# Kernel tuning notes

Hardware: AMD Instinct MI355X
Metric: run time of the kernel (lower is better)

Reference implementation:

```python
import jax, jax.numpy as jnp
import numpy as np

T, HID, H = 1024, 2048, 16
LQ, LKV = 1536, 512
DR, DN, DQ, DV = 64, 128, 192, 128
HI, DI, TOPK = 16, 128, 256
EPS = 1e-6
NEG = -1e30


def _rms(x, g, eps=EPS):
    return x * jax.lax.rsqrt(jnp.mean(x * x, -1, keepdims=True) + eps) * g


def _ln(x, w, b, eps=1e-6):
    m = jnp.mean(x, -1, keepdims=True)
    v = jnp.mean((x - m) ** 2, -1, keepdims=True)
    return (x - m) * jax.lax.rsqrt(v + eps) * w + b


def _rope_interleave(x, cos, sin):
    # HF apply_rotary_pos_emb_interleave: de-interleave even/odd then standard rotate_half.
    x1, x2 = x[..., 0::2], x[..., 1::2]
    xr = jnp.concatenate([x1, x2], -1)
    rot = jnp.concatenate([-x2, x1], -1)
    return xr * cos + rot * sin


def _sparse_indices(hidden, q_lat, cos, sin, ks, ke, i_wqb, i_wk, i_ln_w, i_ln_b, i_wproj):
    # hidden [T,HID], q_lat [T,LQ]; returns [T,TOPK] int32 (sentinel index = T)
    t = hidden.shape[0]
    q_idx = (q_lat @ i_wqb.T).reshape(t, HI, DI)
    k_idx = _ln(hidden @ i_wk.T, i_ln_w, i_ln_b)          # [T,DI]
    w = hidden @ i_wproj.T                                 # [T,HI]
    q_pe = _rope_interleave(q_idx[..., :DR], cos[:, None, :], sin[:, None, :])
    k_pe = _rope_interleave(k_idx[..., :DR], cos, sin)
    qi = jnp.concatenate([q_pe, q_idx[..., DR:]], -1)      # [T,HI,DI]
    ki = jnp.concatenate([k_pe, k_idx[..., DR:]], -1)      # [T,DI]
    weight_scale = DI ** -0.5 * HI ** -0.5
    logits = jnp.einsum('thd,sd->ths', qi, ki)             # [T,HI,T]
    score = jnp.einsum('ths,th->ts', jax.nn.relu(logits), w) * weight_scale
    pos = jnp.arange(t)
    valid = (pos[None, :] >= ks[:, None]) & (pos[None, :] <= ke[:, None])
    score = jnp.where(valid, score, NEG)
    vals, idx = jax.lax.top_k(score, TOPK)
    return jnp.where(vals <= NEG / 2, t, idx).astype(jnp.int32)


def reference(hidden_states, cos, sin, ks, ke,
              w_qa, g_qa, w_qb, w_kva, g_kva, w_kvb, w_o,
              i_wqb, i_wk, i_ln_w, i_ln_b, i_wproj):
    t = hidden_states.shape[1]
    # low-rank projections
    q_lat = _rms(hidden_states @ w_qa.T, g_qa)             # [1,T,LQ]
    ckv = hidden_states @ w_kva.T                          # [1,T,LKV+DR]
    k_c = _rms(ckv[..., :LKV], g_kva)                      # [1,T,LKV]
    k_r = _rope_interleave(ckv[..., LKV:], cos[None], sin[None])  # [1,T,DR]
    # fp8 indexer (reference math in fp32), no-grad in original
    indices = _sparse_indices(hidden_states[0], q_lat[0], cos, sin, ks, ke,
                              i_wqb, i_wk, i_ln_w, i_ln_b, i_wproj)  # [T,TOPK]
    # MLA up-proj with weight absorption
    q_full = (q_lat @ w_qb.T).reshape(1, t, H, DQ)
    q_nope, q_rope = q_full[..., :DN], q_full[..., DN:]
    q_rope = _rope_interleave(q_rope, cos[None, :, None, :], sin[None, :, None, :])
    w_b = w_kvb.reshape(H, DN + DV, LKV)
    w_kn, w_v = w_b[:, :DN, :], w_b[:, DN:, :]
    q_abs = jnp.einsum('bshd,hdk->bshk', q_nope, w_kn)     # absorb k_nope up-proj
    sq = jnp.concatenate([q_abs, q_rope], -1)[0]           # [T,H,LKV+DR]
    skv = jnp.concatenate([k_c, k_r], -1)[0]               # [T,LKV+DR]
    skv = jnp.concatenate([skv, jnp.zeros((1, LKV + DR), skv.dtype)], 0)  # sentinel row
    # sparse attention over gathered top-k KV rows
    kv_g = skv[indices]                                    # [T,TOPK,LKV+DR]
    logits = jnp.einsum('thd,tjd->thj', sq, kv_g) * (DQ ** -0.5)
    logits = jnp.where(indices[:, None, :] == t, NEG, logits)
    p = jax.nn.softmax(logits, -1)
    out = jnp.einsum('thj,tjk->thk', p, kv_g[..., :LKV])   # values = compressed kv
    o = jnp.einsum('thk,hdk->thd', out, w_v)               # un-absorb v up-proj
    return o.reshape(1, t, H * DV) @ w_o.T


def setup_inputs() -> dict:
    key = jax.random.key(0)
    k = jax.random.split(key, 12)
    n = lambda kk, shape, s: jax.random.normal(kk, shape, jnp.float32) * s
    pos = jnp.arange(T, dtype=jnp.float32)
    inv = 1.0 / (10000.0 ** (jnp.arange(0, DR, 2, dtype=jnp.float32) / DR))
    ang = pos[:, None] * inv[None, :]
    cos = jnp.concatenate([jnp.cos(ang), jnp.cos(ang)], -1)
    sin = jnp.concatenate([jnp.sin(ang), jnp.sin(ang)], -1)
    return dict(
        hidden_states=n(k[0], (1, T, HID), 1.0),
        cos=cos, sin=sin,
        ks=jnp.zeros((T,), jnp.int32),
        ke=jnp.arange(T, dtype=jnp.int32),  # causal: keys s <= t valid
        w_qa=n(k[1], (LQ, HID), HID ** -0.5),
        g_qa=jnp.ones((LQ,), jnp.float32),
        w_qb=n(k[2], (H * DQ, LQ), LQ ** -0.5),
        w_kva=n(k[3], (LKV + DR, HID), HID ** -0.5),
        g_kva=jnp.ones((LKV,), jnp.float32),
        w_kvb=n(k[4], (H * (DN + DV), LKV), LKV ** -0.5),
        w_o=n(k[5], (HID, H * DV), (H * DV) ** -0.5),
        i_wqb=n(k[6], (HI * DI, LQ), LQ ** -0.5),
        i_wk=n(k[7], (DI, HID), HID ** -0.5),
        i_ln_w=jnp.ones((DI,), jnp.float32),
        i_ln_b=jnp.zeros((DI,), jnp.float32),
        i_wproj=n(k[8], (HI, HID), HID ** -0.5),
    )
```

## Files before the change

kernel.cpp:

```cpp
#include <hip/hip_runtime.h>
#include <hip/hip_bf16.h>
#include <cmath>

#define T_ 1024
#define HID_ 2048
#define H_ 16
#define LQ_ 1536
#define LKV_ 512
#define DR_ 64
#define DN_ 128
#define DQ_ 192
#define DV_ 128
#define HI_ 16
#define DI_ 128
#define TOPK_ 256
#define NEGF (-1e30f)

typedef short bfrag_t __attribute__((ext_vector_type(8)));
typedef float f32x4 __attribute__((ext_vector_type(4)));

__device__ __forceinline__ float wave_sum64(float v) {
#pragma unroll
  for (int off = 32; off; off >>= 1) v += __shfl_xor(v, off);
  return v;
}

#define GLL(g, l) __builtin_amdgcn_global_load_lds((const __attribute__((address_space(1))) void*)(g), \
                                     (__attribute__((address_space(3))) void*)(l), 16, 0, 0)

__global__ __launch_bounds__(256) void zero_k(float4* __restrict__ p, int n4) {
  int i = blockIdx.x * 256 + threadIdx.x;
  if (i < n4) p[i] = make_float4(0.f, 0.f, 0.f, 0.f);
}

template<typename CT>
__global__ __launch_bounds__(256) void gemm_bf_k(
    const short* __restrict__ A, int lda, long long sA,
    const short* __restrict__ B, int ldb, long long sB,
    CT* __restrict__ C, int ldc, long long sC,
    int Nout, int K)
{
  __shared__ short As[2][128 * 32];
  __shared__ short Bs[2][128 * 32];
  A += (long long)blockIdx.z * sA;
  B += (long long)blockIdx.z * sB;
  C += (long long)blockIdx.z * sC;
  const int tid = threadIdx.x;
  const int bm = blockIdx.y * 128, bn = blockIdx.x * 128;
  const int wave = tid >> 6, lane = tid & 63;
  const int wm = (wave >> 1) * 64, wn = (wave & 1) * 64;
  const int sr = tid >> 2;
  const int scol = (tid & 3) * 8;
  const int m0 = lane & 15, koff = (lane >> 4) * 8;
  f32x4 acc[4][4] = {};
  const short* ga = A + (long long)(bm + sr) * lda + scol;
  const short* gb = B + (long long)(bn + sr) * ldb + scol;
#define STAGE_BF(buf, off) \
    GLL(ga + (off), As[buf] + tid * 8); GLL(ga + (off) + 64 * lda, As[buf] + tid * 8 + 2048); \
    GLL(gb + (off), Bs[buf] + tid * 8); GLL(gb + (off) + 64 * ldb, Bs[buf] + tid * 8 + 2048);
  const int niter = K >> 5;
  STAGE_BF(0, 0);
  for (int it = 0; it < niter; ++it) {
    const int cur = it & 1;
    if (it + 1 < niter) {
      STAGE_BF(cur ^ 1, (it + 1) * 32);
      asm volatile("s_waitcnt vmcnt(4)\ns_barrier" ::: "memory");
    } else {
      asm volatile("s_waitcnt vmcnt(0)\ns_barrier" ::: "memory");
    }
    bfrag_t af[4], bfv[4];
#pragma unroll
    for (int i = 0; i < 4; ++i)
      af[i] = *(const bfrag_t*)(As[cur] + (wm + i * 16 + m0) * 32 + koff);
#pragma unroll
    for (int j = 0; j < 4; ++j)
      bfv[j] = *(const bfrag_t*)(Bs[cur] + (wn + j * 16 + m0) * 32 + koff);
#pragma unroll
    for (int i = 0; i < 4; ++i)
#pragma unroll
      for (int j = 0; j < 4; ++j)
        acc[i][j] = __builtin_amdgcn_mfma_f32_16x16x32_bf16(af[i], bfv[j], acc[i][j], 0, 0, 0);
    asm volatile("s_barrier" ::: "memory");
  }
#undef STAGE_BF
  const int cr = (lane >> 4) * 4, cc = lane & 15;
#pragma unroll
  for (int i = 0; i < 4; ++i) {
    int row = bm + wm + i * 16 + cr;
#pragma unroll
    for (int j = 0; j < 4; ++j) {
      int col = bn + wn + j * 16 + cc;
      if (col < Nout) {
#pragma unroll
        for (int r = 0; r < 4; ++r)
          C[(long long)(row + r) * ldc + col] = (CT)(acc[i][j][r]);
      }
    }
  }
}

__global__ __launch_bounds__(256) void gemm_bfs_k(
    const short* __restrict__ A, int lda,
    const short* __restrict__ B, int ldb,
    float* __restrict__ C, int ldc, int Nout, int K)
{
  __shared__ short As[2][128 * 32];
  __shared__ short Bs[2][128 * 32];
  const long long kbase = (long long)blockIdx.z * K;
  const int tid = threadIdx.x;
  const int bm = blockIdx.y * 128, bn = blockIdx.x * 128;
  const int wave = tid >> 6, lane = tid & 63;
  const int wm = (wave >> 1) * 64, wn = (wave & 1) * 64;
  const int sr = tid >> 2;
  const int scol = (tid & 3) * 8;
  const int m0 = lane & 15, koff = (lane >> 4) * 8;
  f32x4 acc[4][4] = {};
  const short* ga = A + (long long)(bm + sr) * lda + kbase + scol;
  const short* gb = B + (long long)(bn + sr) * ldb + kbase + scol;
#define STAGE_BS(buf, off) \
    GLL(ga + (off), As[buf] + tid * 8); GLL(ga + (off) + 64 * lda, As[buf] + tid * 8 + 2048); \
    GLL(gb + (off), Bs[buf] + tid * 8); GLL(gb + (off) + 64 * ldb, Bs[buf] + tid * 8 + 2048);
  const int niter = K >> 5;
  STAGE_BS(0, 0);
  for (int it = 0; it < niter; ++it) {
    const int cur = it & 1;
    if (it + 1 < niter) {
      STAGE_BS(cur ^ 1, (it + 1) * 32);
      asm volatile("s_waitcnt vmcnt(4)\ns_barrier" ::: "memory");
    } else {
      asm volatile("s_waitcnt vmcnt(0)\ns_barrier" ::: "memory");
    }
    bfrag_t af[4], bfv[4];
#pragma unroll
    for (int i = 0; i < 4; ++i)
      af[i] = *(const bfrag_t*)(As[cur] + (wm + i * 16 + m0) * 32 + koff);
#pragma unroll
    for (int j = 0; j < 4; ++j)
      bfv[j] = *(const bfrag_t*)(Bs[cur] + (wn + j * 16 + m0) * 32 + koff);
#pragma unroll
    for (int i = 0; i < 4; ++i)
#pragma unroll
      for (int j = 0; j < 4; ++j)
        acc[i][j] = __builtin_amdgcn_mfma_f32_16x16x32_bf16(af[i], bfv[j], acc[i][j], 0, 0, 0);
    asm volatile("s_barrier" ::: "memory");
  }
#undef STAGE_BS
  const int cr = (lane >> 4) * 4, cc = lane & 15;
#pragma unroll
  for (int i = 0; i < 4; ++i) {
    int row = bm + wm + i * 16 + cr;
#pragma unroll
    for (int j = 0; j < 4; ++j) {
      int col = bn + wn + j * 16 + cc;
      if (col < Nout) {
#pragma unroll
        for (int r = 0; r < 4; ++r)
          atomicAdd(&C[(long long)(row + r) * ldc + col], acc[i][j][r]);
      }
    }
  }
}

__global__ __launch_bounds__(256) void gemm3_k(
    const short* __restrict__ Ah, const short* __restrict__ Al, int lda,
    const short* __restrict__ Bh, const short* __restrict__ Bl, int ldb,
    float* __restrict__ C, int ldc, int Nout, int K)
{
  __shared__ short Ahs[2][128 * 32];
  __shared__ short Als[2][128 * 32];
  __shared__ short Bhs[2][128 * 32];
  __shared__ short Bls[2][128 * 32];
  const long long kbase = (long long)blockIdx.z * K;
  const int tid = threadIdx.x;
  const int bm = blockIdx.y * 128, bn = blockIdx.x * 128;
  const int wave = tid >> 6, lane = tid & 63;
  const int wm = (wave >> 1) * 64, wn = (wave & 1) * 64;
  const int sr = tid >> 2;
  const int scol = (tid & 3) * 8;
  const int m0 = lane & 15, koff = (lane >> 4) * 8;
  f32x4 acc[4][4] = {};
  const short* gah = Ah + (long long)(bm + sr) * lda + kbase + scol;
  const short* gal = Al + (long long)(bm + sr) * lda + kbase + scol;
  const short* gbh = Bh + (long long)(bn + sr) * ldb + kbase + scol;
  const short* gbl = Bl + (long long)(bn + sr) * ldb + kbase + scol;
#define STAGE_3(buf, off) \
    GLL(gah + (off), Ahs[buf] + tid * 8); GLL(gah + (off) + 64 * lda, Ahs[buf] + tid * 8 + 2048); \
    GLL(gal + (off), Als[buf] + tid * 8); GLL(gal + (off) + 64 * lda, Als[buf] + tid * 8 + 2048); \
    GLL(gbh + (off), Bhs[buf] + tid * 8); GLL(gbh + (off) + 64 * ldb, Bhs[buf] + tid * 8 + 2048); \
    GLL(gbl + (off), Bls[buf] + tid * 8); GLL(gbl + (off) + 64 * ldb, Bls[buf] + tid * 8 + 2048);
  const int niter = K >> 5;
  STAGE_3(0, 0);
  for (int it = 0; it < niter; ++it) {
    const int cur = it & 1;
    if (it + 1 < niter) {
      STAGE_3(cur ^ 1, (it + 1) * 32);
      asm volatile("s_waitcnt vmcnt(8)\ns_barrier" ::: "memory");
    } else {
      asm volatile("s_waitcnt vmcnt(0)\ns_barrier" ::: "memory");
    }
    bfrag_t afh[4], afl[4], bfh[4], bfl[4];
#pragma unroll
    for (int i = 0; i < 4; ++i) {
      afh[i] = *(const bfrag_t*)(Ahs[cur] + (wm + i * 16 + m0) * 32 + koff);
      afl[i] = *(const bfrag_t*)(Als[cur] + (wm + i * 16 + m0) * 32 + koff);
    }
#pragma unroll
    for (int j = 0; j < 4; ++j) {
      bfh[j] = *(const bfrag_t*)(Bhs[cur] + (wn + j * 16 + m0) * 32 + koff);
      bfl[j] = *(const bfrag_t*)(Bls[cur] + (wn + j * 16 + m0) * 32 + koff);
    }
#pragma unroll
    for (int i = 0; i < 4; ++i)
#pragma unroll
      for (int j = 0; j < 4; ++j)
        acc[i][j] = __builtin_amdgcn_mfma_f32_16x16x32_bf16(afh[i], bfh[j], acc[i][j], 0, 0, 0);
#pragma unroll
    for (int i = 0; i < 4; ++i)
#pragma unroll
      for (int j = 0; j < 4; ++j)
        acc[i][j] = __builtin_amdgcn_mfma_f32_16x16x32_bf16(afh[i], bfl[j], acc[i][j], 0, 0, 0);
#pragma unroll
    for (int i = 0; i < 4; ++i)
#pragma unroll
      for (int j = 0; j < 4; ++j)
        acc[i][j] = __builtin_amdgcn_mfma_f32_16x16x32_bf16(afl[i], bfh[j], acc[i][j], 0, 0, 0);
    asm volatile("s_barrier" ::: "memory");
  }
#undef STAGE_3
  const int cr = (lane >> 4) * 4, cc = lane & 15;
  const bool spl = (gridDim.z > 1);
#pragma unroll
  for (int i = 0; i < 4; ++i) {
    int row = bm + wm + i * 16 + cr;
#pragma unroll
    for (int j = 0; j < 4; ++j) {
      int col = bn + wn + j * 16 + cc;
      if (col < Nout) {
#pragma unroll
        for (int r = 0; r < 4; ++r) {
          if (spl) atomicAdd(&C[(long long)(row + r) * ldc + col], acc[i][j][r]);
          else     C[(long long)(row + r) * ldc + col] = acc[i][j][r];
        }
      }
    }
  }
}

__global__ __launch_bounds__(256) void cast_bf16_k(const float* __restrict__ src,
                                                   __hip_bfloat16* __restrict__ dst, int n4) {
  int i = blockIdx.x * 256 + threadIdx.x;
  if (i >= n4) return;
  float4 v = ((const float4*)src)[i];
  union { ushort4 u; __hip_bfloat16 h[4]; } o;
  o.h[0] = __float2bfloat16(v.x); o.h[1] = __float2bfloat16(v.y);
  o.h[2] = __float2bfloat16(v.z); o.h[3] = __float2bfloat16(v.w);
  ((ushort4*)dst)[i] = o.u;
}

__global__ __launch_bounds__(256) void decomp_k(const float* __restrict__ src,
                                                __hip_bfloat16* __restrict__ hi,
                                                __hip_bfloat16* __restrict__ lo, int n4) {
  int i = blockIdx.x * 256 + threadIdx.x;
  if (i >= n4) return;
  float4 v = ((const float4*)src)[i];
  float f[4] = {v.x, v.y, v.z, v.w};
  union { ushort4 u; __hip_bfloat16 h[4]; } oh, ol;
#pragma unroll
  for (int j = 0; j < 4; ++j) {
    __hip_bfloat16 h = __float2bfloat16(f[j]);
    oh.h[j] = h;
    ol.h[j] = __float2bfloat16(f[j] - __bfloat162float(h));
  }
  ((ushort4*)hi)[i] = oh.u;
  ((ushort4*)lo)[i] = ol.u;
}

__global__ __launch_bounds__(256) void cast_pad_k(const float* __restrict__ src,
                                                  __hip_bfloat16* __restrict__ dst,
                                                  int N, int K4, int Npad) {
  int i = blockIdx.x * 256 + threadIdx.x;
  if (i >= Npad * K4) return;
  int r = i / K4;
  float4 v = make_float4(0.f, 0.f, 0.f, 0.f);
  if (r < N) v = ((const float4*)src)[i];
  union { ushort4 u; __hip_bfloat16 h[4]; } o;
  o.h[0] = __float2bfloat16(v.x); o.h[1] = __float2bfloat16(v.y);
  o.h[2] = __float2bfloat16(v.z); o.h[3] = __float2bfloat16(v.w);
  ((ushort4*)dst)[i] = o.u;
}

__global__ __launch_bounds__(256) void wkn_t_k(const float* __restrict__ wkvb,
                                               __hip_bfloat16* __restrict__ dst) {
  __shared__ float tile[64][65];
  const int h = blockIdx.z, k0 = blockIdx.y * 64, d0 = blockIdx.x * 64;
  const int c = threadIdx.x & 63, r0 = threadIdx.x >> 6;
#pragma unroll
  for (int rr = 0; rr < 16; ++rr) {
    int r = r0 + rr * 4;
    tile[r][c] = wkvb[((h * 256 + d0 + r) << 9) + k0 + c];
  }
  __syncthreads();
#pragma unroll
  for (int rr = 0; rr < 16; ++rr) {
    int r = r0 + rr * 4;
    dst[((h * 512 + k0 + r) << 7) + d0 + c] = __float2bfloat16(tile[c][r]);
  }
}

__global__ __launch_bounds__(256) void wv_cast_k(const float* __restrict__ wkvb,
                                                 __hip_bfloat16* __restrict__ dst) {
  int i = blockIdx.x * 256 + threadIdx.x;
  int k = i & 511, dv = (i >> 9) & 127, h = i >> 16;
  dst[i] = __float2bfloat16(wkvb[((h * 256 + 128 + dv) << 9) + k]);
}

__global__ __launch_bounds__(256) void rms_inplace_k(float* x, const float* __restrict__ g,
                                                     int C) {
  int t = blockIdx.x, tid = threadIdx.x;
  float* row = x + (long long)t * C;
  float ss = 0.f;
  for (int i = tid; i < C; i += 256) { float v = row[i]; ss += v * v; }
  __shared__ float red[4];
  ss = wave_sum64(ss);
  if ((tid & 63) == 0) red[tid >> 6] = ss;
  __syncthreads();
  float sc = rsqrtf((red[0] + red[1] + red[2] + red[3]) / (float)C + 1e-6f);
  for (int i = tid; i < C; i += 256) row[i] = row[i] * sc * g[i];
}

__global__ __launch_bounds__(256) void skv_build_k(const float* __restrict__ ckv,
                                                   const float* __restrict__ g,
                                                   const float* __restrict__ cosb,
                                                   const float* __restrict__ sinb,
                                                   __hip_bfloat16* __restrict__ skv) {
  int t = blockIdx.x, tid = threadIdx.x;
  __hip_bfloat16* out = skv + (long long)t * 576;
  if (t == T_) { for (int i = tid; i < 576; i += 256) out[i] = __float2bfloat16(0.f); return; }
  const float* row = ckv + (long long)t * 576;
  float ss = 0.f;
  for (int i = tid; i < 512; i += 256) { float v = row[i]; ss += v * v; }
  __shared__ float red[4];
  ss = wave_sum64(ss);
  if ((tid & 63) == 0) red[tid >> 6] = ss;
  __syncthreads();
  float sc = rsqrtf((red[0] + red[1] + red[2] + red[3]) / 512.f + 1e-6f);
  for (int i = tid; i < 512; i += 256) out[i] = __float2bfloat16(row[i] * sc * g[i]);
  if (tid < 64) {
    int j = tid, j2 = tid & 31;
    float c = cosb[t * 64 + j], s = sinb[t * 64 + j];
    float a = row[512 + 2 * j2], b = row[512 + 2 * j2 + 1];
    out[512 + j] = __float2bfloat16((j < 32) ? (a * c - b * s) : (a * s + b * c));
  }
}

__global__ __launch_bounds__(64) void rope_qi_k(float* qi, const float* __restrict__ cosb,
                                                const float* __restrict__ sinb) {
  int b = blockIdx.x, t = b >> 4, j = threadIdx.x, j2 = j & 31;
  float* x = qi + (long long)b * DI_;
  float c = cosb[t * 64 + j], s = sinb[t * 64 + j];
  float a = x[2 * j2], bb = x[2 * j2 + 1];
  float o = (j < 32) ? (a * c - bb * s) : (a * s + bb * c);
  x[j] = o;
}

__global__ __launch_bounds__(128) void ki_ln_rope_k(float* kbuf, const float* __restrict__ w,
                                                    const float* __restrict__ bia,
                                                    const float* __restrict__ cosb,
                                                    const float* __restrict__ sinb) {
  int t = blockIdx.x, i = threadIdx.x;
  float* row = kbuf + (long long)t * DI_;
  float x = row[i];
  __shared__ float red[2];
  float s1 = wave_sum64(x);
  if ((i & 63) == 0) red[i >> 6] = s1;
  __syncthreads();
  float mean = (red[0] + red[1]) / 128.f;
  float d = x - mean;
  __syncthreads();
  float s2 = wave_sum64(d * d);
  if ((i & 63) == 0) red[i >> 6] = s2;
  __syncthreads();
  float var = (red[0] + red[1]) / 128.f;
  float y = d * rsqrtf(var + 1e-6f) * w[i] + bia[i];
  __shared__ float rowl[128];
  rowl[i] = y;
  __syncthreads();
  float outv = y;
  if (i < 64) {
    int j2 = i & 31;
    float c = cosb[t * 64 + i], s = sinb[t * 64 + i];
    float a = rowl[2 * j2], b = rowl[2 * j2 + 1];
    outv = (i < 32) ? (a * c - b * s) : (a * s + b * c);
  }
  row[i] = outv;
}

__global__ __launch_bounds__(64) void rope_q_sq_k(const __hip_bfloat16* __restrict__ qfull,
                                                  const float* __restrict__ cosb,
                                                  const float* __restrict__ sinb,
                                                  __hip_bfloat16* __restrict__ sq) {
  int b = blockIdx.x, t = b >> 4, h = b & 15, j = threadIdx.x, j2 = j & 31;
  const __hip_bfloat16* x = qfull + (long long)t * 3072 + h * 192 + 128;
  float c = cosb[t * 64 + j], s = sinb[t * 64 + j];
  float a = __bfloat162float(x[2 * j2]), bb = __bfloat162float(x[2 * j2 + 1]);
  float o = (j < 32) ? (a * c - bb * s) : (a * s + bb * c);
  sq[((long long)t * H_ + h) * 576 + 512 + j] = __float2bfloat16(o);
}

__global__ __launch_bounds__(256) void wproj_k(const float* __restrict__ hidden,
                                               const float* __restrict__ wp,
                                               float* __restrict__ out) {
  int wave = threadIdx.x >> 6, lane = threadIdx.x & 63;
  int t = blockIdx.x * 4 + wave;
  const float4* x4 = (const float4*)(hidden + (long long)t * 2048);
  float acc[16] = {};
  for (int c = lane; c < 512; c += 64) {
    float4 xv = x4[c];
#pragma unroll
    for (int h = 0; h < 16; ++h) {
      float4 wv = ((const float4*)(wp + h * 2048))[c];
      acc[h] += xv.x * wv.x + xv.y * wv.y + xv.z * wv.z + xv.w * wv.w;
    }
  }
#pragma unroll
  for (int h = 0; h < 16; ++h) {
    float s = wave_sum64(acc[h]);
    if (lane == 0) out[t * 16 + h] = s;
  }
}

__global__ __launch_bounds__(256) void score_k(
    const short* __restrict__ qi_hi, const short* __restrict__ qi_lo,
    const short* __restrict__ ki_hi, const short* __restrict__ ki_lo,
    const float* __restrict__ wproj, const int* __restrict__ ks,
    const int* __restrict__ ke, float* __restrict__ scores)
{
  __shared__ float s_w[HI_];
  const int seg = blockIdx.x, t = blockIdx.y, tid = threadIdx.x;
  const int wave = tid >> 6, lane = tid & 63;
  const int m0 = lane & 15, quad = lane >> 4;
  if (tid < HI_) s_w[tid] = wproj[t * HI_ + tid] * 0.022097086912079608f;
  __syncthreads();

  bfrag_t ah[4], al[4];
  {
    const short* qh = qi_hi + ((long long)t * HI_ + m0) * DI_ + quad * 8;
    const short* ql = qi_lo + ((long long)t * HI_ + m0) * DI_ + quad * 8;
#pragma unroll
    for (int k = 0; k < 4; ++k) {
      ah[k] = *(const bfrag_t*)(qh + k * 32);
      al[k] = *(const bfrag_t*)(ql + k * 32);
    }
  }
  const int lo = ks[t], hi = ke[t];
  float* srow = scores + t * T_;
#pragma unroll
  for (int tt = 0; tt < 4; ++tt) {
    const int n0 = seg * 256 + wave * 64 + tt * 16;
    const short* kh = ki_hi + (n0 + m0) * DI_ + quad * 8;
    const short* kl = ki_lo + (n0 + m0) * DI_ + quad * 8;
    bfrag_t bh[4], bl[4];
#pragma unroll
    for (int k = 0; k < 4; ++k) {
      bh[k] = *(const bfrag_t*)(kh + k * 32);
      bl[k] = *(const bfrag_t*)(kl + k * 32);
    }
    f32x4 acc = {0.f, 0.f, 0.f, 0.f};
#pragma unroll
    for (int k = 0; k < 4; ++k) {
      acc = __builtin_amdgcn_mfma_f32_16x16x32_bf16(ah[k], bh[k], acc, 0, 0, 0);
      acc = __builtin_amdgcn_mfma_f32_16x16x32_bf16(ah[k], bl[k], acc, 0, 0, 0);
      acc = __builtin_amdgcn_mfma_f32_16x16x32_bf16(al[k], bh[k], acc, 0, 0, 0);
    }
    float sc = 0.f;
#pragma unroll
    for (int r = 0; r < 4; ++r) sc += fmaxf(acc[r], 0.f) * s_w[quad * 4 + r];
    sc += __shfl_xor(sc, 16);
    sc += __shfl_xor(sc, 32);
    if (quad == 0) {
      int key = n0 + m0;
      srow[key] = (key >= lo && key <= hi) ? sc : NEGF;
    }
  }
}

__global__ __launch_bounds__(256) void topk_k(const float* __restrict__ scores,
                                              int* __restrict__ indices)
{
  __shared__ unsigned s_hist[256];
  __shared__ unsigned s_wsum[4];
  __shared__ unsigned s_binsel[2];
  __shared__ unsigned s_cnt;
  const int t = blockIdx.x, tid = threadIdx.x;
  const int wave = tid >> 6, lane = tid & 63;
  const int i0 = tid * 4;
  if (tid == 0) s_cnt = 0;

  float4 sv = ((const float4*)(scores + t * T_))[tid];
  float f[4] = {sv.x, sv.y, sv.z, sv.w};
  unsigned key[4];
#pragma unroll
  for (int j = 0; j < 4; ++j) {
    unsigned u = __float_as_uint(f[j]);
    key[j] = (u & 0x80000000u) ? ~u : (u | 0x80000000u);
  }

  unsigned prefix = 0, Gprev = 0;
  for (int lvl = 0; lvl < 4; ++lvl) {
    const int shift = 24 - 8 * lvl;
    s_hist[tid] = 0;
    __syncthreads();
#pragma unroll
    for (int j = 0; j < 4; ++j) {
      unsigned k = key[j];
      bool part = (lvl == 0) || ((k >> (shift + 8)) == prefix);
      unsigned bin = (k >> shift) & 255u;
      unsigned long long mask = __ballot(part);
#pragma unroll
      for (int b = 0; b < 8; ++b) {
        unsigned long long bal = __ballot((bin >> b) & 1u);
        mask &= ((bin >> b) & 1u) ? bal : ~bal;
      }
      if (part && lane == (__ffsll((long long)mask) - 1))
        atomicAdd(&s_hist[bin], (unsigned)__popcll(mask));
    }
    __syncthreads();
    unsigned h = s_hist[255 - tid];
    unsigned sc_ = h;
    for (int off = 1; off < 64; off <<= 1) {
      unsigned v = __shfl_up(sc_, off);
      if (lane >= off) sc_ += v;
    }
    if (lane == 63) s_wsum[wave] = sc_;
    __syncthreads();
    unsigned wo = 0;
    for (int w = 0; w < wave; ++w) wo += s_wsum[w];
    unsigned incl = sc_ + wo, excl = incl - h;
    unsigned Rn = 256 - Gprev;
    if (excl < Rn && Rn <= incl) { s_binsel[0] = 255 - (unsigned)tid; s_binsel[1] = excl; }
    __syncthreads();
    prefix = (prefix << 8) | s_binsel[0];
    Gprev += s_binsel[1];
  }
  const unsigned thr = prefix;
  const unsigned Rq = 256 - Gprev;
  const unsigned negfkey = ~__float_as_uint(NEGF);

  unsigned eqc = 0;
#pragma unroll
  for (int j = 0; j < 4; ++j) eqc += (key[j] == thr) ? 1u : 0u;
  unsigned esc = eqc;
  for (int off = 1; off < 64; off <<= 1) {
    unsigned v = __shfl_up(esc, off);
    if (lane >= off) esc += v;
  }
  if (lane == 63) s_wsum[wave] = esc;
  __syncthreads();
  unsigned eo = 0;
  for (int w = 0; w < wave; ++w) eo += s_wsum[w];
  unsigned rank = esc + eo - eqc;

#pragma unroll
  for (int j = 0; j < 4; ++j) {
    unsigned k = key[j];
    int outv = (k == negfkey) ? T_ : (i0 + j);
    bool gt = (k > thr);
    unsigned long long bal = __ballot(gt);
    if (bal) {
      int leader = __ffsll((long long)bal) - 1;
      unsigned base = 0;
      if (lane == leader) base = atomicAdd(&s_cnt, (unsigned)__popcll(bal));
      base = (unsigned)__shfl((int)base, leader);
      if (gt) {
        unsigned pre = (unsigned)__popcll(bal & ((1ull << lane) - 1ull));
        indices[t * TOPK_ + base + pre] = outv;
      }
    }
    if (!gt && k == thr) {
      if (rank < Rq) indices[t * TOPK_ + Gprev + rank] = outv;
      rank++;
    }
  }
}

#define SP_LD 257
#define PB_LD 264
#define VT_LD 264
__global__ __launch_bounds__(512) void attn_k(
    const short* __restrict__ sq, const short* __restrict__ skv,
    const int* __restrict__ indices, __hip_bfloat16* __restrict__ attn_out)
{
  __shared__ int s_ind[TOPK_];
  __shared__ __align__(16) char s_un[2 * 64 * VT_LD * 2];
  float* s_p  = (float*)s_un;
  short* s_pb = (short*)(s_un + 16448);
  short* s_vt = (short*)s_un;
  const int t = blockIdx.x, tid = threadIdx.x;
  const int wave = tid >> 6, lane = tid & 63;
  const int m0 = lane & 15, quad = lane >> 4;
  if (tid < TOPK_) s_ind[tid] = indices[t * TOPK_ + tid];
  __syncthreads();

  {
    const int jb = wave * 32;
    int rows[2];
    const short* kvp[2];
#pragma unroll
    for (int j = 0; j < 2; ++j) {
      rows[j] = s_ind[jb + j * 16 + m0];
      kvp[j] = skv + rows[j] * 576 + quad * 8;
    }
    const short* qp = sq + ((long long)t * H_ + m0) * 576 + quad * 8;
    f32x4 qacc[2] = {};
    for (int ks = 0; ks < 18; ++ks) {
      const int k0 = ks * 32;
      bfrag_t aq = *(const bfrag_t*)(qp + k0);
#pragma unroll
      for (int j = 0; j < 2; ++j) {
        bfrag_t bq = *(const bfrag_t*)(kvp[j] + k0);
        qacc[j] = __builtin_amdgcn_mfma_f32_16x16x32_bf16(aq, bq, qacc[j], 0, 0, 0);
      }
    }
    const float scale = 0.07216878364870322f;
#pragma unroll
    for (int j = 0; j < 2; ++j) {
      int key = jb + j * 16 + m0;
      bool msk = (rows[j] == T_);
#pragma unroll
      for (int r = 0; r < 4; ++r)
        s_p[(quad * 4 + r) * SP_LD + key] = msk ? NEGF : qacc[j][r] * scale;
    }
  }
  __syncthreads();

  for (int h = wave * 2; h < wave * 2 + 2; ++h) {
    float* ph = s_p + h * SP_LD;
    float m = -3.4e38f;
    for (int j = lane; j < TOPK_; j += 64) m = fmaxf(m, ph[j]);
#pragma unroll
    for (int off = 32; off; off >>= 1) m = fmaxf(m, __shfl_xor(m, off));
    float sum = 0.f;
    for (int j = lane; j < TOPK_; j += 64) {
      float e = __expf(ph[j] - m);
      ph[j] = e; sum += e;
    }
    sum = wave_sum64(sum);
    float inv = 1.f / sum;
    for (int j = lane; j < TOPK_; j += 64) ph[j] *= inv;
  }
  __syncthreads();

  {
    const int col = tid & 255, h0 = tid >> 8;
#pragma unroll
    for (int h = 0; h < 8; ++h) {
      const int hh = h0 + h * 2;
      s_pb[hh * PB_LD + col] =
          (short)__bfloat16_as_ushort(__float2bfloat16(s_p[hh * SP_LD + col]));
    }
  }
  __syncthreads();

  bfrag_t apf[8];
#pragma unroll
  for (int kk = 0; kk < 8; ++kk)
    apf[kk] = *(const bfrag_t*)(s_pb + m0 * PB_LD + kk * 32 + quad * 8);

  const int grp = wave >> 2, gw = wave & 3;
  short* svt = s_vt + grp * (64 * VT_LD);
  const int r8 = (tid >> 3) & 31;
  const int bb = tid & 7;

  for (int cc = 0; cc < 4; ++cc) {
    const int c = grp * 4 + cc;
    __syncthreads();
#pragma unroll
    for (int rep = 0; rep < 8; ++rep) {
      const int kv = r8 + 32 * rep;
      const int row = s_ind[kv];
      bfrag_t v = *(const bfrag_t*)(skv + (long long)row * 576 + c * 64 + bb * 8);
      const int colx = kv ^ (bb << 3);
#pragma unroll
      for (int j = 0; j < 8; ++j)
        svt[(bb * 8 + j) * VT_LD + colx] = v[j];
    }
    __syncthreads();
    const int d = gw * 16 + m0;
    const short* vrow = svt + d * VT_LD;
    const int sx = (d >> 3) << 3;
    f32x4 oacc = {0.f, 0.f, 0.f, 0.f};
#pragma unroll
    for (int kk = 0; kk < 8; ++kk) {
      bfrag_t bv = *(const bfrag_t*)(vrow + ((kk * 32 + quad * 8) ^ sx));
      oacc = __builtin_amdgcn_mfma_f32_16x16x32_bf16(apf[kk], bv, oacc, 0, 0, 0);
    }
    const int col = c * 64 + d;
#pragma unroll
    for (int r = 0; r < 4; ++r)
      attn_out[((long long)t * H_ + quad * 4 + r) * 512 + col] = __float2bfloat16(oacc[r]);
  }
}

extern "C" void kernel_launch(void* const* d_in, const int* in_sizes, int n_in,
                              void* d_out, int out_size, void* d_ws, size_t ws_size,
                              hipStream_t stream) {
  const float* hidden  = (const float*)d_in[0];
  const float* cosb    = (const float*)d_in[1];
  const float* sinb    = (const float*)d_in[2];
  const int*   ks      = (const int*)d_in[3];
  const int*   ke      = (const int*)d_in[4];
  const float* w_qa    = (const float*)d_in[5];
  const float* g_qa    = (const float*)d_in[6];
  const float* w_qb    = (const float*)d_in[7];
  const float* w_kva   = (const float*)d_in[8];
  const float* g_kva   = (const float*)d_in[9];
  const float* w_kvb   = (const float*)d_in[10];
  const float* w_o     = (const float*)d_in[11];
  const float* i_wqb   = (const float*)d_in[12];
  const float* i_wk    = (const float*)d_in[13];
  const float* i_ln_w  = (const float*)d_in[14];
  const float* i_ln_b  = (const float*)d_in[15];
  const float* i_wproj = (const float*)d_in[16];
  float* out = (float*)d_out;
  (void)in_sizes; (void)n_in; (void)out_size; (void)ws_size;

  char* ws = (char*)d_ws;
  __hip_bfloat16* hid_hi  = (__hip_bfloat16*)(ws + 0);
  __hip_bfloat16* hid_lo  = (__hip_bfloat16*)(ws + 4194304);
  float*          q_lat   = (float*)(ws + 8388608);
  __hip_bfloat16* qi_hi   = (__hip_bfloat16*)(ws + 8388608);
  __hip_bfloat16* qlat_hi = (__hip_bfloat16*)(ws + 14680064);
  __hip_bfloat16* qlat_lo = (__hip_bfloat16*)(ws + 17825792);
  float*          qi      = (float*)(ws + 20971520);
  float*          scoresb = (float*)(ws + 20971520);
  float*          kib     = (float*)(ws + 29360128);
  float*          wbuf    = (float*)(ws + 29884416);
  float*          ckv     = (float*)(ws + 29949952);
  __hip_bfloat16* qi_lo   = (__hip_bfloat16*)(ws + 29949952);
  __hip_bfloat16* ki_hi   = (__hip_bfloat16*)(ws + 34144256);
  __hip_bfloat16* ki_lo   = (__hip_bfloat16*)(ws + 34406400);
  __hip_bfloat16* sq_bf   = (__hip_bfloat16*)(ws + 0);
  __hip_bfloat16* o_bf    = (__hip_bfloat16*)(ws + 0);
  __hip_bfloat16* W       = (__hip_bfloat16*)(ws + 37748736);
  __hip_bfloat16* skv_bf  = (__hip_bfloat16*)(ws + 47185920);
  int*            idxb    = (int*)(ws + 48366720);
  __hip_bfloat16* E       = (__hip_bfloat16*)(ws + 49415296);

  dim3 blk(256);
  const short* Ws = (const short*)W;
  const short* Es = (const short*)E;

  decomp_k<<<2048, blk, 0, stream>>>(hidden, hid_hi, hid_lo, 524288);

  decomp_k<<<3072, blk, 0, stream>>>(w_qa, W, E, 786432);
  zero_k<<<1536, blk, 0, stream>>>((float4*)q_lat, 393216);
  gemm3_k<<<dim3(12, 8, 4), blk, 0, stream>>>(
      (const short*)hid_hi, (const short*)hid_lo, HID_, Ws, Es, HID_, q_lat, LQ_, LQ_, 512);
  rms_inplace_k<<<T_, blk, 0, stream>>>(q_lat, g_qa, LQ_);

  cast_pad_k<<<1280, blk, 0, stream>>>(w_kva, W, 576, 512, 640);
  zero_k<<<576, blk, 0, stream>>>((float4*)ckv, 147456);
  gemm_bfs_k<<<dim3(5, 8, 4), blk, 0, stream>>>(
      (const short*)hid_hi, HID_, Ws, HID_, ckv, 576, 576, 512);
  skv_build_k<<<T_ + 1, blk, 0, stream>>>(ckv, g_kva, cosb, sinb, skv_bf);

  decomp_k<<<1536, blk, 0, stream>>>(q_lat, qlat_hi, qlat_lo, 393216);

  decomp_k<<<3072, blk, 0, stream>>>(i_wqb, W, E, 786432);
  zero_k<<<2048, blk, 0, stream>>>((float4*)qi, 524288);
  gemm3_k<<<dim3(16, 8, 4), blk, 0, stream>>>(
      (const short*)qlat_hi, (const short*)qlat_lo, LQ_, Ws, Es, LQ_, qi, HI_ * DI_, HI_ * DI_, 384);
  rope_qi_k<<<T_ * HI_, dim3(64), 0, stream>>>(qi, cosb, sinb);
  decomp_k<<<2048, blk, 0, stream>>>(qi, qi_hi, qi_lo, 524288);

  decomp_k<<<256, blk, 0, stream>>>(i_wk, W, E, 65536);
  zero_k<<<128, blk, 0, stream>>>((float4*)kib, 32768);
  gemm3_k<<<dim3(1, 8, 16), blk, 0, stream>>>(
      (const short*)hid_hi, (const short*)hid_lo, HID_, Ws, Es, HID_, kib, DI_, DI_, 128);
  ki_ln_rope_k<<<T_, dim3(128), 0, stream>>>(kib, i_ln_w, i_ln_b, cosb, sinb);
  decomp_k<<<128, blk, 0, stream>>>(kib, ki_hi, ki_lo, 32768);

  wproj_k<<<256, blk, 0, stream>>>(hidden, i_wproj, wbuf);

  score_k<<<dim3(4, T_), blk, 0, stream>>>(
      (const short*)qi_hi, (const short*)qi_lo, (const short*)ki_hi, (const short*)ki_lo,
      wbuf, ks, ke, scoresb);
  topk_k<<<T_, blk, 0, stream>>>(scoresb, idxb);

  cast_bf16_k<<<4608, blk, 0, stream>>>(w_qb, W, 1179648);
  gemm_bf_k<__hip_bfloat16><<<dim3(24, 8, 1), blk, 0, stream>>>(
      (const short*)qlat_hi, LQ_, 0, Ws, LQ_, 0, (__hip_bfloat16*)E, H_ * DQ_, 0, H_ * DQ_, LQ_);
  rope_q_sq_k<<<T_ * H_, dim3(64), 0, stream>>>(E, cosb, sinb, sq_bf);

  wkn_t_k<<<dim3(2, 8, 16), blk, 0, stream>>>(w_kvb, W);
  gemm_bf_k<__hip_bfloat16><<<dim3(4, 8, 16), blk, 0, stream>>>(
      Es, H_ * DQ_, 192, Ws, DI_, 65536, sq_bf, H_ * 576, 576, LKV_, DN_);

  attn_k<<<T_, dim3(512), 0, stream>>>((const short*)sq_bf, (const short*)skv_bf, idxb, E);

  wv_cast_k<<<4096, blk, 0, stream>>>(w_kvb, W);
  gemm_bf_k<__hip_bfloat16><<<dim3(1, 8, 16), blk, 0, stream>>>(
      Es, H_ * LKV_, 512, Ws, LKV_, 65536, o_bf, H_ * DV_, 128, DV_, LKV_);

  cast_bf16_k<<<4096, blk, 0, stream>>>(w_o, W, 1048576);
  zero_k<<<2048, blk, 0, stream>>>((float4*)out, 524288);
  gemm_bfs_k<<<dim3(16, 8, 4), blk, 0, stream>>>(
      (const short*)o_bf, H_ * DV_, Ws, H_ * DV_, out, HID_, HID_, 512);
}
```

Before: 594.3 us.

## Restructure indexer score kernel as LDS-tiled 128x128 split-bf16 GEMM

Replaces the per-token score kernel, which reloaded the whole key matrix from global memory for every token, with a tiled GEMM. Each block covers a 128x128 tile (8 tokens x 16 heads by 128 keys), stages hi/lo operands through double-buffered LDS with async global-to-LDS loads, and fuses the ReLU, head-weighted sum and causal mask into the epilogue. This is meant to cut redundant global and L2 traffic and raise MFMA utilization, at the cost of much more LDS per block, which may lower occupancy.

```diff
diff --git a/kernel.cpp b/kernel.cpp
--- a/kernel.cpp
+++ b/kernel.cpp
@@ -246,6 +246,100 @@
   }
 }
 
+__global__ __launch_bounds__(256) void score_gemm_k(
+    const short* __restrict__ Ah, const short* __restrict__ Al,
+    const short* __restrict__ Bh, const short* __restrict__ Bl,
+    const float* __restrict__ wproj, const int* __restrict__ ks,
+    const int* __restrict__ ke, float* __restrict__ scores)
+{
+  __shared__ short Ahs[2][128 * 32];
+  __shared__ short Als[2][128 * 32];
+  __shared__ short Bhs[2][128 * 32];
+  __shared__ short Bls[2][128 * 32];
+  __shared__ float s_w[8][16];
+  __shared__ int s_ks[8], s_ke[8];
+  const int tid = threadIdx.x;
+  const int bm = blockIdx.y * 128, bn = blockIdx.x * 128;
+  const int wave = tid >> 6, lane = tid & 63;
+  const int wm = (wave >> 1) * 64, wn = (wave & 1) * 64;
+  const int sr = tid >> 2;
+  const int scol = (tid & 3) * 8;
+  const int m0 = lane & 15, koff = (lane >> 4) * 8;
+  const int t0 = bm >> 4;
+  if (tid < 128) s_w[tid >> 4][tid & 15] =
+      wproj[(t0 + (tid >> 4)) * HI_ + (tid & 15)] * 0.022097086912079608f;
+  if (tid < 8) { s_ks[tid] = ks[t0 + tid]; s_ke[tid] = ke[t0 + tid]; }
+  f32x4 acc[4][4] = {};
+  const short* gah = Ah + (long long)(bm + sr) * DI_ + scol;
+  const short* gal = Al + (long long)(bm + sr) * DI_ + scol;
+  const short* gbh = Bh + (long long)(bn + sr) * DI_ + scol;
+  const short* gbl = Bl + (long long)(bn + sr) * DI_ + scol;
+#define STAGE_S(buf, off) \
+    GLL(gah + (off), Ahs[buf] + tid * 8); GLL(gah + (off) + 64 * DI_, Ahs[buf] + tid * 8 + 2048); \
+    GLL(gal + (off), Als[buf] + tid * 8); GLL(gal + (off) + 64 * DI_, Als[buf] + tid * 8 + 2048); \
+    GLL(gbh + (off), Bhs[buf] + tid * 8); GLL(gbh + (off) + 64 * DI_, Bhs[buf] + tid * 8 + 2048); \
+    GLL(gbl + (off), Bls[buf] + tid * 8); GLL(gbl + (off) + 64 * DI_, Bls[buf] + tid * 8 + 2048);
+  const int niter = DI_ >> 5;
+  STAGE_S(0, 0);
+  for (int it = 0; it < niter; ++it) {
+    const int cur = it & 1;
+    if (it + 1 < niter) {
+      STAGE_S(cur ^ 1, (it + 1) * 32);
+      asm volatile("s_waitcnt vmcnt(8)\ns_barrier" ::: "memory");
+    } else {
+      asm volatile("s_waitcnt vmcnt(0)\ns_barrier" ::: "memory");
+    }
+    bfrag_t afh[4], afl[4], bfh[4], bfl[4];
+#pragma unroll
+    for (int i = 0; i < 4; ++i) {
+      afh[i] = *(const bfrag_t*)(Ahs[cur] + (wm + i * 16 + m0) * 32 + koff);
+      afl[i] = *(const bfrag_t*)(Als[cur] + (wm + i * 16 + m0) * 32 + koff);
+    }
+#pragma unroll
+    for (int j = 0; j < 4; ++j) {
+      bfh[j] = *(const bfrag_t*)(Bhs[cur] + (wn + j * 16 + m0) * 32 + koff);
+      bfl[j] = *(const bfrag_t*)(Bls[cur] + (wn + j * 16 + m0) * 32 + koff);
+    }
+#pragma unroll
+    for (int i = 0; i < 4; ++i)
+#pragma unroll
+      for (int j = 0; j < 4; ++j)
+        acc[i][j] = __builtin_amdgcn_mfma_f32_16x16x32_bf16(afh[i], bfh[j], acc[i][j], 0, 0, 0);
+#pragma unroll
+    for (int i = 0; i < 4; ++i)
+#pragma unroll
+      for (int j = 0; j < 4; ++j)
+        acc[i][j] = __builtin_amdgcn_mfma_f32_16x16x32_bf16(afh[i], bfl[j], acc[i][j], 0, 0, 0);
+#pragma unroll
+    for (int i = 0; i < 4; ++i)
+#pragma unroll
+      for (int j = 0; j < 4; ++j)
+        acc[i][j] = __builtin_amdgcn_mfma_f32_16x16x32_bf16(afl[i], bfh[j], acc[i][j], 0, 0, 0);
+    asm volatile("s_barrier" ::: "memory");
+  }
+#undef STAGE_S
+  const int cc = lane & 15, quad = lane >> 4;
+#pragma unroll
+  for (int i = 0; i < 4; ++i) {
+    const int g = (wm >> 4) + i;
+    const int tok = t0 + g;
+    const int lo = s_ks[g], hi = s_ke[g];
+#pragma unroll
+    for (int j = 0; j < 4; ++j) {
+      float sc = 0.f;
+#pragma unroll
+      for (int r = 0; r < 4; ++r)
+        sc += fmaxf(acc[i][j][r], 0.f) * s_w[g][quad * 4 + r];
+      sc += __shfl_xor(sc, 16);
+      sc += __shfl_xor(sc, 32);
+      if (quad == 0) {
+        const int s = bn + wn + j * 16 + cc;
+        scores[tok * T_ + s] = (s >= lo && s <= hi) ? sc : NEGF;
+      }
+    }
+  }
+}
+
 __global__ __launch_bounds__(256) void cast_bf16_k(const float* __restrict__ src,
                                                    __hip_bfloat16* __restrict__ dst, int n4) {
   int i = blockIdx.x * 256 + threadIdx.x;
@@ -426,61 +520,6 @@
   for (int h = 0; h < 16; ++h) {
     float s = wave_sum64(acc[h]);
     if (lane == 0) out[t * 16 + h] = s;
-  }
-}
-
-__global__ __launch_bounds__(256) void score_k(
-    const short* __restrict__ qi_hi, const short* __restrict__ qi_lo,
-    const short* __restrict__ ki_hi, const short* __restrict__ ki_lo,
-    const float* __restrict__ wproj, const int* __restrict__ ks,
-    const int* __restrict__ ke, float* __restrict__ scores)
-{
-  __shared__ float s_w[HI_];
-  const int seg = blockIdx.x, t = blockIdx.y, tid = threadIdx.x;
-  const int wave = tid >> 6, lane = tid & 63;
-  const int m0 = lane & 15, quad = lane >> 4;
-  if (tid < HI_) s_w[tid] = wproj[t * HI_ + tid] * 0.022097086912079608f;
-  __syncthreads();
-
-  bfrag_t ah[4], al[4];
-  {
-    const short* qh = qi_hi + ((long long)t * HI_ + m0) * DI_ + quad * 8;
-    const short* ql = qi_lo + ((long long)t * HI_ + m0) * DI_ + quad * 8;
-#pragma unroll
-    for (int k = 0; k < 4; ++k) {
-      ah[k] = *(const bfrag_t*)(qh + k * 32);
-      al[k] = *(const bfrag_t*)(ql + k * 32);
-    }
-  }
-  const int lo = ks[t], hi = ke[t];
-  float* srow = scores + t * T_;
-#pragma unroll
-  for (int tt = 0; tt < 4; ++tt) {
-    const int n0 = seg * 256 + wave * 64 + tt * 16;
-    const short* kh = ki_hi + (n0 + m0) * DI_ + quad * 8;
-    const short* kl = ki_lo + (n0 + m0) * DI_ + quad * 8;
-    bfrag_t bh[4], bl[4];
-#pragma unroll
-    for (int k = 0; k < 4; ++k) {
-      bh[k] = *(const bfrag_t*)(kh + k * 32);
-      bl[k] = *(const bfrag_t*)(kl + k * 32);
-    }
-    f32x4 acc = {0.f, 0.f, 0.f, 0.f};
-#pragma unroll
-    for (int k = 0; k < 4; ++k) {
-      acc = __builtin_amdgcn_mfma_f32_16x16x32_bf16(ah[k], bh[k], acc, 0, 0, 0);
-      acc = __builtin_amdgcn_mfma_f32_16x16x32_bf16(ah[k], bl[k], acc, 0, 0, 0);
-      acc = __builtin_amdgcn_mfma_f32_16x16x32_bf16(al[k], bh[k], acc, 0, 0, 0);
-    }
-    float sc = 0.f;
-#pragma unroll
-    for (int r = 0; r < 4; ++r) sc += fmaxf(acc[r], 0.f) * s_w[quad * 4 + r];
-    sc += __shfl_xor(sc, 16);
-    sc += __shfl_xor(sc, 32);
-    if (quad == 0) {
-      int key = n0 + m0;
-      srow[key] = (key >= lo && key <= hi) ? sc : NEGF;
-    }
   }
 }
 
@@ -782,7 +821,7 @@
 
   wproj_k<<<256, blk, 0, stream>>>(hidden, i_wproj, wbuf);
 
-  score_k<<<dim3(4, T_), blk, 0, stream>>>(
+  score_gemm_k<<<dim3(8, 128), blk, 0, stream>>>(
       (const short*)qi_hi, (const short*)qi_lo, (const short*)ki_hi, (const short*)ki_lo,
       wbuf, ks, ke, scoresb);
   topk_k<<<T_, blk, 0, stream>>>(scoresb, idxb);
```

Result: faster. 542.6 us (-8.7%).
